# Kernel tuning notes

Measured on AMD Instinct MI355X. Metric: run time of the kernel, lower is better.

The kernel has to match this reference:

```python
import jax, jax.numpy as jnp
import numpy as np
import math

B, S, D = 16, 2048, 128

def setup_inputs() -> dict:
    key = jax.random.key(0)
    k1, k2, k3, k4 = jax.random.split(key, 4)
    query = jax.random.normal(k1, (B, S, D), dtype=jnp.float32)
    key_t = jax.random.normal(k2, (B, S, D), dtype=jnp.float32)
    value = jax.random.normal(k3, (B, S, D), dtype=jnp.float32)
    attn_mask = jax.random.randint(k4, (B, S, S), 0, 2).astype(bool)
    return {"query": query, "key": key_t, "value": value, "attn_mask": attn_mask}

def reference(query, key, value, attn_mask):
    # score = Q K^T / sqrt(d)  -> [B, Sq, Sk]
    scale = 1.0 / math.sqrt(query.shape[-1])
    score = jnp.einsum('bqd,bkd->bqk', query, key) * scale
    # faithful quirk: masked positions are replaced by the VALUE 1e-9 (not -inf)
    mask_score = jnp.where(attn_mask, jnp.float32(1e-9), score)
    # faithful quirk: softmax over dim=1 (the query axis), as in the torch source
    score_matrix = jax.nn.softmax(mask_score, axis=1)
    # output = softmax(scores) @ V  -> [B, Sq, D]
    output = jnp.einsum('bqk,bkd->bqd', score_matrix, value)
    return output
```

## Files before the change

kernel.cpp:

```cpp
#include <hip/hip_runtime.h>
#include <math.h>

#define NB 16
#define SS 2048
#define DQ 128
#define SCALE 0.08838834764831845f

typedef __bf16 bf16x8 __attribute__((ext_vector_type(8)));
typedef unsigned short ushort8_t __attribute__((ext_vector_type(8)));
typedef float floatx4 __attribute__((ext_vector_type(4)));

__device__ __forceinline__ unsigned short f2bf(float x) {
  unsigned int u = __float_as_uint(x);
  u += 0x7fffu + ((u >> 16) & 1u);
  return (unsigned short)(u >> 16);
}
union FragU { ushort8_t u; bf16x8 b; };
__device__ __forceinline__ bf16x8 ld_frag(const unsigned short* p) {
  FragU t; t.u = *(const ushort8_t*)p; return t.b;
}
__device__ __forceinline__ floatx4 mfma16(bf16x8 a, bf16x8 b, floatx4 c) {
  return __builtin_amdgcn_mfma_f32_16x16x32_bf16(a, b, c, 0, 0, 0);
}

__device__ __forceinline__ void bar_lds() {
  asm volatile("s_waitcnt lgkmcnt(0)\n\ts_barrier" ::: "memory");
}


__global__ void zero_accum(float* __restrict__ O) {
  float* p = O + (size_t)blockIdx.x * SS * DQ + 16 * DQ;
#pragma unroll
  for (int i = 0; i < 8; ++i) p[threadIdx.x + 256 * i] = 0.f;
}

template<int WRITE_E>
__global__ __launch_bounds__(256, 4) void pass1_colsum(
    const float* __restrict__ Q, const float* __restrict__ K,
    const int* __restrict__ M, float* __restrict__ O,
    unsigned short* __restrict__ E)
{
  const int k0  = blockIdx.x * 64;
  const int b   = blockIdx.y;
  const int qc  = blockIdx.z;
  const int tid = threadIdx.x;
  const int w = tid >> 6, lane = tid & 63, l15 = lane & 15, quad = lane >> 4;

  __shared__ unsigned short Kbf[64][136];
  __shared__ unsigned short Qbf[64][136];
  __shared__ float red[4][64];

  const float* Qb = Q + (size_t)b * SS * DQ;
  const float* Kb = K + (size_t)b * SS * DQ;
  const int*   Mb = M + (size_t)b * SS * SS;
  unsigned short* Eb = WRITE_E ? (E + (size_t)b * SS * SS) : nullptr;

  const int srow = tid >> 5;
  const int sc4  = (tid & 31) * 4;

#pragma unroll
  for (int r = 0; r < 8; ++r) {
    int row = srow + r * 8;
    float4 v = *(const float4*)(Kb + (size_t)(k0 + row) * DQ + sc4);
    *(ushort4*)&Kbf[row][sc4] = make_ushort4(f2bf(v.x), f2bf(v.y), f2bf(v.z), f2bf(v.w));
  }

  const int qlane = 16 * w + l15;

  float4 qreg[8];
  int4 mv_nxt[4];
  {
    const int q0 = qc * 512;
#pragma unroll
    for (int r = 0; r < 8; ++r)
      qreg[r] = *(const float4*)(Qb + (size_t)(q0 + srow + r * 8) * DQ + sc4);
#pragma unroll
    for (int i = 0; i < 4; ++i)
      mv_nxt[i] = *(const int4*)(Mb + (size_t)(q0 + qlane) * SS + k0 + 16 * i + quad * 4);
  }

  float colacc[16];
#pragma unroll
  for (int t = 0; t < 16; ++t) colacc[t] = 0.f;

  for (int qi = 0; qi < 8; ++qi) {
    bar_lds();
    int4 mv[4] = {mv_nxt[0], mv_nxt[1], mv_nxt[2], mv_nxt[3]};
#pragma unroll
    for (int r = 0; r < 8; ++r) {
      float4 v = qreg[r];
      *(ushort4*)&Qbf[srow + r * 8][sc4] =
          make_ushort4(f2bf(v.x), f2bf(v.y), f2bf(v.z), f2bf(v.w));
    }
    bar_lds();
    if (qi < 7) {
      const int qn = qc * 512 + (qi + 1) * 64;
#pragma unroll
      for (int r = 0; r < 8; ++r)
        qreg[r] = *(const float4*)(Qb + (size_t)(qn + srow + r * 8) * DQ + sc4);
#pragma unroll
      for (int i = 0; i < 4; ++i)
        mv_nxt[i] = *(const int4*)(Mb + (size_t)(qn + qlane) * SS + k0 + 16 * i + quad * 4);
    }

    floatx4 acc[4];
#pragma unroll
    for (int i = 0; i < 4; ++i) acc[i] = (floatx4){0.f, 0.f, 0.f, 0.f};
#pragma unroll
    for (int d0 = 0; d0 < DQ; d0 += 32) {
      bf16x8 bq = ld_frag(&Qbf[qlane][d0 + quad * 8]);
#pragma unroll
      for (int i = 0; i < 4; ++i) {
        bf16x8 ak = ld_frag(&Kbf[16 * i + l15][d0 + quad * 8]);
        acc[i] = mfma16(ak, bq, acc[i]);
      }
    }
    const int qrow = qc * 512 + qi * 64 + qlane;
#pragma unroll
    for (int i = 0; i < 4; ++i) {
      int mm[4] = {mv[i].x, mv[i].y, mv[i].z, mv[i].w};
      float ev[4];
#pragma unroll
      for (int r = 0; r < 4; ++r) {
        float s = mm[r] ? 1e-9f : acc[i][r] * SCALE;
        ev[r] = __expf(s);
        colacc[i * 4 + r] += ev[r];
      }
      if (WRITE_E) {
        *(ushort4*)(Eb + (size_t)qrow * SS + k0 + 16 * i + quad * 4) =
            make_ushort4(f2bf(ev[0]), f2bf(ev[1]), f2bf(ev[2]), f2bf(ev[3]));
      }
    }
  }

#pragma unroll
  for (int t = 0; t < 16; ++t) {
    colacc[t] += __shfl_xor(colacc[t], 1, 64);
    colacc[t] += __shfl_xor(colacc[t], 2, 64);
    colacc[t] += __shfl_xor(colacc[t], 4, 64);
    colacc[t] += __shfl_xor(colacc[t], 8, 64);
  }
  if (l15 == 0) {
#pragma unroll
    for (int i = 0; i < 4; ++i)
#pragma unroll
      for (int r = 0; r < 4; ++r)
        red[w][16 * i + quad * 4 + r] = colacc[i * 4 + r];
  }
  bar_lds();
  if (tid < 64) {
    float s = red[0][tid] + red[1][tid] + red[2][tid] + red[3][tid];
    atomicAdd(O + (size_t)b * SS * DQ + 16 * DQ + k0 + tid, s);
  }
}

__global__ void combine_linv(float* __restrict__ O) {
  const int b  = blockIdx.x;
  const int jb = blockIdx.y * 4;
  float* Ob = O + (size_t)b * SS * DQ;
#pragma unroll
  for (int it = 0; it < 8; ++it) {
    int k = threadIdx.x + 256 * it;
    float inv = 1.0f / Ob[16 * DQ + k];
#pragma unroll
    for (int j = 0; j < 4; ++j)
      Ob[(size_t)(64 * (jb + j)) * DQ + k] = inv;
  }
}

__global__ __launch_bounds__(256, 2) void pass2_pv(
    const float* __restrict__ V, const unsigned short* __restrict__ E,
    float* __restrict__ O)
{
  const int b = blockIdx.y, q0 = blockIdx.x * 64;
  const int tid = threadIdx.x;
  const int w = tid >> 6, lane = tid & 63, l15 = lane & 15, quad = lane >> 4;

  __shared__ unsigned short Wt[128][72];
  __shared__ float Li[SS];

  const float* Vb = V + (size_t)b * SS * DQ;
  const unsigned short* Erow =
      E + (size_t)b * SS * SS + (size_t)(q0 + 16 * w + l15) * SS;

  const int sc4 = (tid & 31) * 4;
  const int vk2 = (tid >> 5) * 2;

  {
    const float* src = O + ((size_t)b * SS + q0) * DQ;
#pragma unroll
    for (int r = 0; r < 2; ++r) {
      int idx = (tid + r * 256) * 4;
      *(float4*)&Li[idx] = *(const float4*)(src + idx);
    }
  }

  floatx4 accO[8];
#pragma unroll
  for (int j = 0; j < 8; ++j) accO[j] = (floatx4){0.f, 0.f, 0.f, 0.f};

  float4 vreg[8];
  FragU ef_nxt[2];
  {
#pragma unroll
    for (int r = 0; r < 4; ++r) {
      int k2 = vk2 + r * 16;
      vreg[2 * r]     = *(const float4*)(Vb + (size_t)(k2)     * DQ + sc4);
      vreg[2 * r + 1] = *(const float4*)(Vb + (size_t)(k2 + 1) * DQ + sc4);
    }
#pragma unroll
    for (int c = 0; c < 2; ++c)
      ef_nxt[c].u = *(const ushort8_t*)(Erow + 32 * c + quad * 8);
  }

  for (int k0 = 0; k0 < SS; k0 += 64) {
    bar_lds();
    FragU ef[2] = {ef_nxt[0], ef_nxt[1]};

#pragma unroll
    for (int r = 0; r < 4; ++r) {
      int k2 = vk2 + r * 16;
      float la = Li[k0 + k2], lb = Li[k0 + k2 + 1];
      float fa[4] = {vreg[2*r].x * la, vreg[2*r].y * la,
                     vreg[2*r].z * la, vreg[2*r].w * la};
      float fb[4] = {vreg[2*r+1].x * lb, vreg[2*r+1].y * lb,
                     vreg[2*r+1].z * lb, vreg[2*r+1].w * lb};
#pragma unroll
      for (int i = 0; i < 4; ++i) {
        int d  = sc4 + i;
        int kk = k2 ^ ((((unsigned)d >> 2) & 7) << 3);
        *(ushort2*)&Wt[d][kk] = make_ushort2(f2bf(fa[i]), f2bf(fb[i]));
      }
    }
    bar_lds();

    if (k0 + 64 < SS) {
      const int kn = k0 + 64;
#pragma unroll
      for (int r = 0; r < 4; ++r) {
        int k2 = vk2 + r * 16;
        vreg[2 * r]     = *(const float4*)(Vb + (size_t)(kn + k2)     * DQ + sc4);
        vreg[2 * r + 1] = *(const float4*)(Vb + (size_t)(kn + k2 + 1) * DQ + sc4);
      }
#pragma unroll
      for (int c = 0; c < 2; ++c)
        ef_nxt[c].u = *(const ushort8_t*)(Erow + kn + 32 * c + quad * 8);
    }

#pragma unroll
    for (int c = 0; c < 2; ++c) {
      bf16x8 be = ef[c].b;
#pragma unroll
      for (int j = 0; j < 8; ++j) {
        int d  = 16 * j + l15;
        int kk = (32 * c + quad * 8) ^ ((((unsigned)d >> 2) & 7) << 3);
        bf16x8 aw = ld_frag(&Wt[d][kk]);
        accO[j] = mfma16(aw, be, accO[j]);
      }
    }
  }

#pragma unroll
  for (int j = 0; j < 8; ++j) {
    float* op = O + ((size_t)b * SS + q0 + 16 * w + l15) * DQ + 16 * j + quad * 4;
    *(float4*)op = make_float4(accO[j][0], accO[j][1], accO[j][2], accO[j][3]);
  }
}

__global__ __launch_bounds__(256, 2) void pass2_out(
    const float* __restrict__ Q, const float* __restrict__ K,
    const float* __restrict__ V, const int* __restrict__ M,
    float* __restrict__ O)
{
  const int b = blockIdx.y, q0 = blockIdx.x * 64;
  const int tid = threadIdx.x;
  const int w = tid >> 6, lane = tid & 63, l15 = lane & 15, quad = lane >> 4;

  __shared__ unsigned short Kbf[64][136];
  __shared__ unsigned short Es[64][72];
  __shared__ unsigned short Wt[128][72];
  __shared__ float Li[SS];

  const float* Qb = Q + (size_t)b * SS * DQ;
  const float* Kb = K + (size_t)b * SS * DQ;
  const float* Vb = V + (size_t)b * SS * DQ;
  const int*   Mb = M + (size_t)b * SS * SS;

  const int srow = tid >> 5;
  const int sc4  = (tid & 31) * 4;

  {
    const float* src = O + ((size_t)b * SS + q0) * DQ;
#pragma unroll
    for (int r = 0; r < 2; ++r) {
      int idx = (tid + r * 256) * 4;
      *(float4*)&Li[idx] = *(const float4*)(src + idx);
    }
  }
  FragU qf[4];
  {
    const float* qrow = Qb + (size_t)(q0 + 16 * w + l15) * DQ;
#pragma unroll
    for (int i = 0; i < 4; ++i) {
      float4 a = *(const float4*)(qrow + 32 * i + quad * 8);
      float4 c = *(const float4*)(qrow + 32 * i + quad * 8 + 4);
      qf[i].u = (ushort8_t){f2bf(a.x), f2bf(a.y), f2bf(a.z), f2bf(a.w),
                            f2bf(c.x), f2bf(c.y), f2bf(c.z), f2bf(c.w)};
    }
  }

  floatx4 accO[8];
#pragma unroll
  for (int j = 0; j < 8; ++j) accO[j] = (floatx4){0.f, 0.f, 0.f, 0.f};

  const int* mrow = Mb + (size_t)(q0 + 16 * w + l15) * SS;

  float4 kreg[8], vreg[8];
  int4 mv_nxt[4];
  const int vk2 = (tid >> 5) * 2;
  {
#pragma unroll
    for (int r = 0; r < 8; ++r)
      kreg[r] = *(const float4*)(Kb + (size_t)(srow + r * 8) * DQ + sc4);
#pragma unroll
    for (int r = 0; r < 4; ++r) {
      int k2 = vk2 + r * 16;
      vreg[2 * r]     = *(const float4*)(Vb + (size_t)(k2)     * DQ + sc4);
      vreg[2 * r + 1] = *(const float4*)(Vb + (size_t)(k2 + 1) * DQ + sc4);
    }
#pragma unroll
    for (int j = 0; j < 4; ++j)
      mv_nxt[j] = *(const int4*)(mrow + 16 * j + quad * 4);
  }

  for (int k0 = 0; k0 < SS; k0 += 64) {
    bar_lds();
    int4 mv[4] = {mv_nxt[0], mv_nxt[1], mv_nxt[2], mv_nxt[3]};

#pragma unroll
    for (int r = 0; r < 8; ++r) {
      float4 v = kreg[r];
      *(ushort4*)&Kbf[srow + r * 8][sc4] =
          make_ushort4(f2bf(v.x), f2bf(v.y), f2bf(v.z), f2bf(v.w));
    }
#pragma unroll
    for (int r = 0; r < 4; ++r) {
      int k2 = vk2 + r * 16;
      float fa[4] = {vreg[2*r].x, vreg[2*r].y, vreg[2*r].z, vreg[2*r].w};
      float fb[4] = {vreg[2*r+1].x, vreg[2*r+1].y, vreg[2*r+1].z, vreg[2*r+1].w};
#pragma unroll
      for (int i = 0; i < 4; ++i) {
        int d  = sc4 + i;
        int kk = k2 ^ ((((unsigned)d >> 2) & 7) << 3);
        *(ushort2*)&Wt[d][kk] = make_ushort2(f2bf(fa[i]), f2bf(fb[i]));
      }
    }
    bar_lds();

    if (k0 + 64 < SS) {
      const int kn = k0 + 64;
#pragma unroll
      for (int r = 0; r < 8; ++r)
        kreg[r] = *(const float4*)(Kb + (size_t)(kn + srow + r * 8) * DQ + sc4);
#pragma unroll
      for (int r = 0; r < 4; ++r) {
        int k2 = vk2 + r * 16;
        vreg[2 * r]     = *(const float4*)(Vb + (size_t)(kn + k2)     * DQ + sc4);
        vreg[2 * r + 1] = *(const float4*)(Vb + (size_t)(kn + k2 + 1) * DQ + sc4);
      }
#pragma unroll
      for (int j = 0; j < 4; ++j)
        mv_nxt[j] = *(const int4*)(mrow + kn + 16 * j + quad * 4);
    }

    floatx4 acc[4];
#pragma unroll
    for (int j = 0; j < 4; ++j) acc[j] = (floatx4){0.f, 0.f, 0.f, 0.f};
#pragma unroll
    for (int i = 0; i < 4; ++i) {
      bf16x8 bq = qf[i].b;
#pragma unroll
      for (int j = 0; j < 4; ++j) {
        bf16x8 ak = ld_frag(&Kbf[16 * j + l15][32 * i + quad * 8]);
        acc[j] = mfma16(ak, bq, acc[j]);
      }
    }
#pragma unroll
    for (int j = 0; j < 4; ++j) {
      float4 liv = *(const float4*)&Li[k0 + 16 * j + quad * 4];
      float lv[4] = {liv.x, liv.y, liv.z, liv.w};
      int mm[4] = {mv[j].x, mv[j].y, mv[j].z, mv[j].w};
      unsigned short es[4];
#pragma unroll
      for (int r = 0; r < 4; ++r) {
        float s = mm[r] ? 1e-9f : acc[j][r] * SCALE;
        es[r] = f2bf(__expf(s) * lv[r]);
      }
      *(ushort4*)&Es[16 * w + l15][16 * j + quad * 4] =
          make_ushort4(es[0], es[1], es[2], es[3]);
    }
#pragma unroll
    for (int c = 0; c < 2; ++c) {
      bf16x8 be = ld_frag(&Es[16 * w + l15][32 * c + quad * 8]);
#pragma unroll
      for (int j = 0; j < 8; ++j) {
        int d  = 16 * j + l15;
        int kk = (32 * c + quad * 8) ^ ((((unsigned)d >> 2) & 7) << 3);
        bf16x8 aw = ld_frag(&Wt[d][kk]);
        accO[j] = mfma16(aw, be, accO[j]);
      }
    }
  }

#pragma unroll
  for (int j = 0; j < 8; ++j) {
    float* op = O + ((size_t)b * SS + q0 + 16 * w + l15) * DQ + 16 * j + quad * 4;
    *(float4*)op = make_float4(accO[j][0], accO[j][1], accO[j][2], accO[j][3]);
  }
}

extern "C" void kernel_launch(void* const* d_in, const int* in_sizes, int n_in,
                              void* d_out, int out_size, void* d_ws, size_t ws_size,
                              hipStream_t stream) {
  const float* Q = (const float*)d_in[0];
  const float* K = (const float*)d_in[1];
  const float* V = (const float*)d_in[2];
  const int*   M = (const int*)d_in[3];
  float* O = (float*)d_out;

  const size_t eneed = (size_t)NB * SS * SS * sizeof(unsigned short);

  zero_accum<<<dim3(NB), 256, 0, stream>>>(O);
  if (d_ws != nullptr && ws_size >= eneed) {
    unsigned short* E = (unsigned short*)d_ws;
    pass1_colsum<1><<<dim3(32, NB, 4), 256, 0, stream>>>(Q, K, M, O, E);
    combine_linv<<<dim3(NB, 8), 256, 0, stream>>>(O);
    pass2_pv<<<dim3(32, NB), 256, 0, stream>>>(V, E, O);
  } else {
    pass1_colsum<0><<<dim3(32, NB, 4), 256, 0, stream>>>(Q, K, M, O, nullptr);
    combine_linv<<<dim3(NB, 8), 256, 0, stream>>>(O);
    pass2_out<<<dim3(32, NB), 256, 0, stream>>>(Q, K, V, M, O);
  }
}
```

Baseline: 513.5 us.

## Split PV pass over two key halves and keep Q fragments in registers

```diff
diff --git a/kernel.cpp b/kernel.cpp
--- a/kernel.cpp
+++ b/kernel.cpp
@@ -47,7 +47,6 @@
   const int w = tid >> 6, lane = tid & 63, l15 = lane & 15, quad = lane >> 4;
 
   __shared__ unsigned short Kbf[64][136];
-  __shared__ unsigned short Qbf[64][136];
   __shared__ float red[4][64];
 
   const float* Qb = Q + (size_t)b * SS * DQ;
@@ -64,70 +63,80 @@
     float4 v = *(const float4*)(Kb + (size_t)(k0 + row) * DQ + sc4);
     *(ushort4*)&Kbf[row][sc4] = make_ushort4(f2bf(v.x), f2bf(v.y), f2bf(v.z), f2bf(v.w));
   }
+  bar_lds();
 
   const int qlane = 16 * w + l15;
+  const float* qrowp = Qb + (size_t)(qc * 512 + qlane) * DQ;
+  const int*   mrowp = Mb + (size_t)(qc * 512 + qlane) * SS + k0;
 
   float4 qreg[8];
   int4 mv_nxt[4];
-  {
-    const int q0 = qc * 512;
-#pragma unroll
-    for (int r = 0; r < 8; ++r)
-      qreg[r] = *(const float4*)(Qb + (size_t)(q0 + srow + r * 8) * DQ + sc4);
-#pragma unroll
-    for (int i = 0; i < 4; ++i)
-      mv_nxt[i] = *(const int4*)(Mb + (size_t)(q0 + qlane) * SS + k0 + 16 * i + quad * 4);
-  }
+#pragma unroll
+  for (int i = 0; i < 4; ++i) {
+    qreg[2 * i]     = *(const float4*)(qrowp + 32 * i + quad * 8);
+    qreg[2 * i + 1] = *(const float4*)(qrowp + 32 * i + quad * 8 + 4);
+  }
+#pragma unroll
+  for (int j = 0; j < 4; ++j)
+    mv_nxt[j] = *(const int4*)(mrowp + 16 * j + quad * 4);
 
   float colacc[16];
 #pragma unroll
   for (int t = 0; t < 16; ++t) colacc[t] = 0.f;
 
   for (int qi = 0; qi < 8; ++qi) {
-    bar_lds();
-    int4 mv[4] = {mv_nxt[0], mv_nxt[1], mv_nxt[2], mv_nxt[3]};
-#pragma unroll
-    for (int r = 0; r < 8; ++r) {
-      float4 v = qreg[r];
-      *(ushort4*)&Qbf[srow + r * 8][sc4] =
-          make_ushort4(f2bf(v.x), f2bf(v.y), f2bf(v.z), f2bf(v.w));
-    }
-    bar_lds();
+    FragU qf[4];
+#pragma unroll
+    for (int i = 0; i < 4; ++i) {
+      float4 a = qreg[2 * i], c = qreg[2 * i + 1];
+      qf[i].u = (ushort8_t){f2bf(a.x), f2bf(a.y), f2bf(a.z), f2bf(a.w),
+                            f2bf(c.x), f2bf(c.y), f2bf(c.z), f2bf(c.w)};
+    }
+    int mbits = 0;
+#pragma unroll
+    for (int j = 0; j < 4; ++j) {
+      mbits |= (mv_nxt[j].x ? 1 : 0) << (4 * j + 0);
+      mbits |= (mv_nxt[j].y ? 1 : 0) << (4 * j + 1);
+      mbits |= (mv_nxt[j].z ? 1 : 0) << (4 * j + 2);
+      mbits |= (mv_nxt[j].w ? 1 : 0) << (4 * j + 3);
+    }
     if (qi < 7) {
-      const int qn = qc * 512 + (qi + 1) * 64;
-#pragma unroll
-      for (int r = 0; r < 8; ++r)
-        qreg[r] = *(const float4*)(Qb + (size_t)(qn + srow + r * 8) * DQ + sc4);
-#pragma unroll
-      for (int i = 0; i < 4; ++i)
-        mv_nxt[i] = *(const int4*)(Mb + (size_t)(qn + qlane) * SS + k0 + 16 * i + quad * 4);
+      const float* qp = qrowp + (size_t)(qi + 1) * 64 * DQ;
+      const int*   mp = mrowp + (size_t)(qi + 1) * 64 * SS;
+#pragma unroll
+      for (int i = 0; i < 4; ++i) {
+        qreg[2 * i]     = *(const float4*)(qp + 32 * i + quad * 8);
+        qreg[2 * i + 1] = *(const float4*)(qp + 32 * i + quad * 8 + 4);
+      }
+#pragma unroll
+      for (int j = 0; j < 4; ++j)
+        mv_nxt[j] = *(const int4*)(mp + 16 * j + quad * 4);
     }
 
     floatx4 acc[4];
 #pragma unroll
-    for (int i = 0; i < 4; ++i) acc[i] = (floatx4){0.f, 0.f, 0.f, 0.f};
-#pragma unroll
-    for (int d0 = 0; d0 < DQ; d0 += 32) {
-      bf16x8 bq = ld_frag(&Qbf[qlane][d0 + quad * 8]);
-#pragma unroll
-      for (int i = 0; i < 4; ++i) {
-        bf16x8 ak = ld_frag(&Kbf[16 * i + l15][d0 + quad * 8]);
-        acc[i] = mfma16(ak, bq, acc[i]);
+    for (int j = 0; j < 4; ++j) acc[j] = (floatx4){0.f, 0.f, 0.f, 0.f};
+#pragma unroll
+    for (int i = 0; i < 4; ++i) {
+      bf16x8 bq = qf[i].b;
+#pragma unroll
+      for (int j = 0; j < 4; ++j) {
+        bf16x8 ak = ld_frag(&Kbf[16 * j + l15][32 * i + quad * 8]);
+        acc[j] = mfma16(ak, bq, acc[j]);
       }
     }
     const int qrow = qc * 512 + qi * 64 + qlane;
 #pragma unroll
-    for (int i = 0; i < 4; ++i) {
-      int mm[4] = {mv[i].x, mv[i].y, mv[i].z, mv[i].w};
+    for (int j = 0; j < 4; ++j) {
       float ev[4];
 #pragma unroll
       for (int r = 0; r < 4; ++r) {
-        float s = mm[r] ? 1e-9f : acc[i][r] * SCALE;
+        float s = ((mbits >> (4 * j + r)) & 1) ? 1e-9f : acc[j][r] * SCALE;
         ev[r] = __expf(s);
-        colacc[i * 4 + r] += ev[r];
+        colacc[j * 4 + r] += ev[r];
       }
       if (WRITE_E) {
-        *(ushort4*)(Eb + (size_t)qrow * SS + k0 + 16 * i + quad * 4) =
+        *(ushort4*)(Eb + (size_t)qrow * SS + k0 + 16 * j + quad * 4) =
             make_ushort4(f2bf(ev[0]), f2bf(ev[1]), f2bf(ev[2]), f2bf(ev[3]));
       }
     }
@@ -168,31 +177,29 @@
   }
 }
 
-__global__ __launch_bounds__(256, 2) void pass2_pv(
+__global__ __launch_bounds__(256, 4) void pass2_pv(
     const float* __restrict__ V, const unsigned short* __restrict__ E,
-    float* __restrict__ O)
+    const float* __restrict__ O, float* __restrict__ P)
 {
-  const int b = blockIdx.y, q0 = blockIdx.x * 64;
+  const int b = blockIdx.z, q0 = blockIdx.x * 64, kh = blockIdx.y;
+  const int kbase = kh * (SS / 2);
   const int tid = threadIdx.x;
   const int w = tid >> 6, lane = tid & 63, l15 = lane & 15, quad = lane >> 4;
 
   __shared__ unsigned short Wt[128][72];
-  __shared__ float Li[SS];
+  __shared__ float Li[SS / 2];
 
   const float* Vb = V + (size_t)b * SS * DQ;
   const unsigned short* Erow =
-      E + (size_t)b * SS * SS + (size_t)(q0 + 16 * w + l15) * SS;
+      E + (size_t)b * SS * SS + (size_t)(q0 + 16 * w + l15) * SS + kbase;
 
   const int sc4 = (tid & 31) * 4;
   const int vk2 = (tid >> 5) * 2;
 
   {
-    const float* src = O + ((size_t)b * SS + q0) * DQ;
-#pragma unroll
-    for (int r = 0; r < 2; ++r) {
-      int idx = (tid + r * 256) * 4;
-      *(float4*)&Li[idx] = *(const float4*)(src + idx);
-    }
+    const float* src = O + ((size_t)b * SS + q0) * DQ + kbase;
+    int idx = tid * 4;
+    *(float4*)&Li[idx] = *(const float4*)(src + idx);
   }
 
   floatx4 accO[8];
@@ -205,15 +212,15 @@
 #pragma unroll
     for (int r = 0; r < 4; ++r) {
       int k2 = vk2 + r * 16;
-      vreg[2 * r]     = *(const float4*)(Vb + (size_t)(k2)     * DQ + sc4);
-      vreg[2 * r + 1] = *(const float4*)(Vb + (size_t)(k2 + 1) * DQ + sc4);
+      vreg[2 * r]     = *(const float4*)(Vb + (size_t)(kbase + k2)     * DQ + sc4);
+      vreg[2 * r + 1] = *(const float4*)(Vb + (size_t)(kbase + k2 + 1) * DQ + sc4);
     }
 #pragma unroll
     for (int c = 0; c < 2; ++c)
       ef_nxt[c].u = *(const ushort8_t*)(Erow + 32 * c + quad * 8);
   }
 
-  for (int k0 = 0; k0 < SS; k0 += 64) {
+  for (int k0 = 0; k0 < SS / 2; k0 += 64) {
     bar_lds();
     FragU ef[2] = {ef_nxt[0], ef_nxt[1]};
 
@@ -234,13 +241,13 @@
     }
     bar_lds();
 
-    if (k0 + 64 < SS) {
+    if (k0 + 64 < SS / 2) {
       const int kn = k0 + 64;
 #pragma unroll
       for (int r = 0; r < 4; ++r) {
         int k2 = vk2 + r * 16;
-        vreg[2 * r]     = *(const float4*)(Vb + (size_t)(kn + k2)     * DQ + sc4);
-        vreg[2 * r + 1] = *(const float4*)(Vb + (size_t)(kn + k2 + 1) * DQ + sc4);
+        vreg[2 * r]     = *(const float4*)(Vb + (size_t)(kbase + kn + k2)     * DQ + sc4);
+        vreg[2 * r + 1] = *(const float4*)(Vb + (size_t)(kbase + kn + k2 + 1) * DQ + sc4);
       }
 #pragma unroll
       for (int c = 0; c < 2; ++c)
@@ -262,8 +269,23 @@
 
 #pragma unroll
   for (int j = 0; j < 8; ++j) {
-    float* op = O + ((size_t)b * SS + q0 + 16 * w + l15) * DQ + 16 * j + quad * 4;
+    float* op = P + (((size_t)(kh * NB + b) * SS) + q0 + 16 * w + l15) * DQ
+                  + 16 * j + quad * 4;
     *(float4*)op = make_float4(accO[j][0], accO[j][1], accO[j][2], accO[j][3]);
+  }
+}
+
+__global__ void combine_O(const float* __restrict__ P, float* __restrict__ O) {
+  const size_t boff = (size_t)blockIdx.x * SS * DQ + (size_t)blockIdx.y * 8192;
+  const float* P0 = P + boff;
+  const float* P1 = P + (size_t)NB * SS * DQ + boff;
+  float* Ob = O + boff;
+#pragma unroll
+  for (int it = 0; it < 8; ++it) {
+    int i = (threadIdx.x + 256 * it) * 4;
+    float4 a = *(const float4*)(P0 + i);
+    float4 c = *(const float4*)(P1 + i);
+    *(float4*)(Ob + i) = make_float4(a.x + c.x, a.y + c.y, a.z + c.z, a.w + c.w);
   }
 }
 
@@ -429,13 +451,16 @@
   float* O = (float*)d_out;
 
   const size_t eneed = (size_t)NB * SS * SS * sizeof(unsigned short);
+  const size_t pneed = eneed + (size_t)2 * NB * SS * DQ * sizeof(float);
 
   zero_accum<<<dim3(NB), 256, 0, stream>>>(O);
-  if (d_ws != nullptr && ws_size >= eneed) {
+  if (d_ws != nullptr && ws_size >= pneed) {
     unsigned short* E = (unsigned short*)d_ws;
+    float* P = (float*)((char*)d_ws + eneed);
     pass1_colsum<1><<<dim3(32, NB, 4), 256, 0, stream>>>(Q, K, M, O, E);
     combine_linv<<<dim3(NB, 8), 256, 0, stream>>>(O);
-    pass2_pv<<<dim3(32, NB), 256, 0, stream>>>(V, E, O);
+    pass2_pv<<<dim3(32, 2, NB), 256, 0, stream>>>(V, E, O, P);
+    combine_O<<<dim3(NB, 32), 256, 0, stream>>>(P, O);
   } else {
     pass1_colsum<0><<<dim3(32, NB, 4), 256, 0, stream>>>(Q, K, M, O, nullptr);
     combine_linv<<<dim3(NB, 8), 256, 0, stream>>>(O);
```

Measured after the change: 603.8 us. +17.6%, slower.

## Split PV pass over key halves and fuse reciprocal into PV load

Applied to the files above, without the earlier changes.

```diff
diff --git a/kernel.cpp b/kernel.cpp
--- a/kernel.cpp
+++ b/kernel.cpp
@@ -168,31 +168,33 @@
   }
 }
 
-__global__ __launch_bounds__(256, 2) void pass2_pv(
+__global__ __launch_bounds__(256, 4) void pass2_pv(
     const float* __restrict__ V, const unsigned short* __restrict__ E,
-    float* __restrict__ O)
+    const float* __restrict__ O, float* __restrict__ P)
 {
-  const int b = blockIdx.y, q0 = blockIdx.x * 64;
+  const int b = blockIdx.z, q0 = blockIdx.x * 64, kh = blockIdx.y;
+  const int kbase = kh * (SS / 2);
   const int tid = threadIdx.x;
   const int w = tid >> 6, lane = tid & 63, l15 = lane & 15, quad = lane >> 4;
 
   __shared__ unsigned short Wt[128][72];
-  __shared__ float Li[SS];
+  __shared__ float Li[SS / 2];
 
   const float* Vb = V + (size_t)b * SS * DQ;
   const unsigned short* Erow =
-      E + (size_t)b * SS * SS + (size_t)(q0 + 16 * w + l15) * SS;
+      E + (size_t)b * SS * SS + (size_t)(q0 + 16 * w + l15) * SS + kbase;
 
   const int sc4 = (tid & 31) * 4;
   const int vk2 = (tid >> 5) * 2;
 
   {
-    const float* src = O + ((size_t)b * SS + q0) * DQ;
-#pragma unroll
-    for (int r = 0; r < 2; ++r) {
-      int idx = (tid + r * 256) * 4;
-      *(float4*)&Li[idx] = *(const float4*)(src + idx);
-    }
+    const float* src = O + (size_t)b * SS * DQ + 16 * DQ + kbase;
+    int idx = tid * 4;
+    float4 c = *(const float4*)(src + idx);
+    Li[idx + 0] = 1.0f / c.x;
+    Li[idx + 1] = 1.0f / c.y;
+    Li[idx + 2] = 1.0f / c.z;
+    Li[idx + 3] = 1.0f / c.w;
   }
 
   floatx4 accO[8];
@@ -205,15 +207,15 @@
 #pragma unroll
     for (int r = 0; r < 4; ++r) {
       int k2 = vk2 + r * 16;
-      vreg[2 * r]     = *(const float4*)(Vb + (size_t)(k2)     * DQ + sc4);
-      vreg[2 * r + 1] = *(const float4*)(Vb + (size_t)(k2 + 1) * DQ + sc4);
+      vreg[2 * r]     = *(const float4*)(Vb + (size_t)(kbase + k2)     * DQ + sc4);
+      vreg[2 * r + 1] = *(const float4*)(Vb + (size_t)(kbase + k2 + 1) * DQ + sc4);
     }
 #pragma unroll
     for (int c = 0; c < 2; ++c)
       ef_nxt[c].u = *(const ushort8_t*)(Erow + 32 * c + quad * 8);
   }
 
-  for (int k0 = 0; k0 < SS; k0 += 64) {
+  for (int k0 = 0; k0 < SS / 2; k0 += 64) {
     bar_lds();
     FragU ef[2] = {ef_nxt[0], ef_nxt[1]};
 
@@ -234,13 +236,13 @@
     }
     bar_lds();
 
-    if (k0 + 64 < SS) {
+    if (k0 + 64 < SS / 2) {
       const int kn = k0 + 64;
 #pragma unroll
       for (int r = 0; r < 4; ++r) {
         int k2 = vk2 + r * 16;
-        vreg[2 * r]     = *(const float4*)(Vb + (size_t)(kn + k2)     * DQ + sc4);
-        vreg[2 * r + 1] = *(const float4*)(Vb + (size_t)(kn + k2 + 1) * DQ + sc4);
+        vreg[2 * r]     = *(const float4*)(Vb + (size_t)(kbase + kn + k2)     * DQ + sc4);
+        vreg[2 * r + 1] = *(const float4*)(Vb + (size_t)(kbase + kn + k2 + 1) * DQ + sc4);
       }
 #pragma unroll
       for (int c = 0; c < 2; ++c)
@@ -262,8 +264,23 @@
 
 #pragma unroll
   for (int j = 0; j < 8; ++j) {
-    float* op = O + ((size_t)b * SS + q0 + 16 * w + l15) * DQ + 16 * j + quad * 4;
+    float* op = P + (((size_t)(kh * NB + b) * SS) + q0 + 16 * w + l15) * DQ
+                  + 16 * j + quad * 4;
     *(float4*)op = make_float4(accO[j][0], accO[j][1], accO[j][2], accO[j][3]);
+  }
+}
+
+__global__ void combine_O(const float* __restrict__ P, float* __restrict__ O) {
+  const size_t boff = (size_t)blockIdx.x * SS * DQ + (size_t)blockIdx.y * 8192;
+  const float* P0 = P + boff;
+  const float* P1 = P + (size_t)NB * SS * DQ + boff;
+  float* Ob = O + boff;
+#pragma unroll
+  for (int it = 0; it < 8; ++it) {
+    int i = (threadIdx.x + 256 * it) * 4;
+    float4 a = *(const float4*)(P0 + i);
+    float4 c = *(const float4*)(P1 + i);
+    *(float4*)(Ob + i) = make_float4(a.x + c.x, a.y + c.y, a.z + c.z, a.w + c.w);
   }
 }
 
@@ -429,13 +446,15 @@
   float* O = (float*)d_out;
 
   const size_t eneed = (size_t)NB * SS * SS * sizeof(unsigned short);
+  const size_t pneed = eneed + (size_t)2 * NB * SS * DQ * sizeof(float);
 
   zero_accum<<<dim3(NB), 256, 0, stream>>>(O);
-  if (d_ws != nullptr && ws_size >= eneed) {
+  if (d_ws != nullptr && ws_size >= pneed) {
     unsigned short* E = (unsigned short*)d_ws;
+    float* P = (float*)((char*)d_ws + eneed);
     pass1_colsum<1><<<dim3(32, NB, 4), 256, 0, stream>>>(Q, K, M, O, E);
-    combine_linv<<<dim3(NB, 8), 256, 0, stream>>>(O);
-    pass2_pv<<<dim3(32, NB), 256, 0, stream>>>(V, E, O);
+    pass2_pv<<<dim3(32, 2, NB), 256, 0, stream>>>(V, E, O, P);
+    combine_O<<<dim3(NB, 32), 256, 0, stream>>>(P, O);
   } else {
     pass1_colsum<0><<<dim3(32, NB, 4), 256, 0, stream>>>(Q, K, M, O, nullptr);
     combine_linv<<<dim3(NB, 8), 256, 0, stream>>>(O);
```

New measurement: 524.1 us. 1.02x slower.

## Swap pass1 loop to keep Q fragments in registers and stream K tiles

Applied to the files above, without the earlier changes.

```diff
diff --git a/kernel.cpp b/kernel.cpp
--- a/kernel.cpp
+++ b/kernel.cpp
@@ -40,117 +40,113 @@
     const int* __restrict__ M, float* __restrict__ O,
     unsigned short* __restrict__ E)
 {
-  const int k0  = blockIdx.x * 64;
+  const int qs  = blockIdx.x * 64;
   const int b   = blockIdx.y;
-  const int qc  = blockIdx.z;
+  const int kc0 = blockIdx.z * 512;
   const int tid = threadIdx.x;
   const int w = tid >> 6, lane = tid & 63, l15 = lane & 15, quad = lane >> 4;
 
   __shared__ unsigned short Kbf[64][136];
-  __shared__ unsigned short Qbf[64][136];
-  __shared__ float red[4][64];
-
-  const float* Qb = Q + (size_t)b * SS * DQ;
+  __shared__ float Csum[4][512];
+
   const float* Kb = K + (size_t)b * SS * DQ;
-  const int*   Mb = M + (size_t)b * SS * SS;
-  unsigned short* Eb = WRITE_E ? (E + (size_t)b * SS * SS) : nullptr;
+  const int qrow = qs + 16 * w + l15;
+
+  const int*   mrow = M + (size_t)b * SS * SS + (size_t)qrow * SS + kc0;
+  unsigned short* Ep =
+      WRITE_E ? (E + (size_t)b * SS * SS + (size_t)qrow * SS + kc0) : nullptr;
 
   const int srow = tid >> 5;
   const int sc4  = (tid & 31) * 4;
 
-#pragma unroll
-  for (int r = 0; r < 8; ++r) {
-    int row = srow + r * 8;
-    float4 v = *(const float4*)(Kb + (size_t)(k0 + row) * DQ + sc4);
-    *(ushort4*)&Kbf[row][sc4] = make_ushort4(f2bf(v.x), f2bf(v.y), f2bf(v.z), f2bf(v.w));
-  }
-
-  const int qlane = 16 * w + l15;
-
-  float4 qreg[8];
+  FragU qf[4];
+  {
+    const float* qp = Q + (size_t)b * SS * DQ + (size_t)qrow * DQ;
+#pragma unroll
+    for (int i = 0; i < 4; ++i) {
+      float4 a = *(const float4*)(qp + 32 * i + quad * 8);
+      float4 c = *(const float4*)(qp + 32 * i + quad * 8 + 4);
+      qf[i].u = (ushort8_t){f2bf(a.x), f2bf(a.y), f2bf(a.z), f2bf(a.w),
+                            f2bf(c.x), f2bf(c.y), f2bf(c.z), f2bf(c.w)};
+    }
+  }
+
+#pragma unroll
+  for (int t = 0; t < 8; ++t) Csum[w][lane + 64 * t] = 0.f;
+
+  float4 kreg[8];
   int4 mv_nxt[4];
-  {
-    const int q0 = qc * 512;
-#pragma unroll
-    for (int r = 0; r < 8; ++r)
-      qreg[r] = *(const float4*)(Qb + (size_t)(q0 + srow + r * 8) * DQ + sc4);
-#pragma unroll
-    for (int i = 0; i < 4; ++i)
-      mv_nxt[i] = *(const int4*)(Mb + (size_t)(q0 + qlane) * SS + k0 + 16 * i + quad * 4);
-  }
-
-  float colacc[16];
-#pragma unroll
-  for (int t = 0; t < 16; ++t) colacc[t] = 0.f;
-
-  for (int qi = 0; qi < 8; ++qi) {
+#pragma unroll
+  for (int r = 0; r < 8; ++r)
+    kreg[r] = *(const float4*)(Kb + (size_t)(kc0 + srow + r * 8) * DQ + sc4);
+#pragma unroll
+  for (int j = 0; j < 4; ++j)
+    mv_nxt[j] = *(const int4*)(mrow + 16 * j + quad * 4);
+
+  for (int kt = 0; kt < 8; ++kt) {
+    const int kbl = kt * 64;
     bar_lds();
     int4 mv[4] = {mv_nxt[0], mv_nxt[1], mv_nxt[2], mv_nxt[3]};
 #pragma unroll
     for (int r = 0; r < 8; ++r) {
-      float4 v = qreg[r];
-      *(ushort4*)&Qbf[srow + r * 8][sc4] =
+      float4 v = kreg[r];
+      *(ushort4*)&Kbf[srow + r * 8][sc4] =
           make_ushort4(f2bf(v.x), f2bf(v.y), f2bf(v.z), f2bf(v.w));
     }
     bar_lds();
-    if (qi < 7) {
-      const int qn = qc * 512 + (qi + 1) * 64;
+    if (kt < 7) {
+      const int kn = kbl + 64;
 #pragma unroll
       for (int r = 0; r < 8; ++r)
-        qreg[r] = *(const float4*)(Qb + (size_t)(qn + srow + r * 8) * DQ + sc4);
-#pragma unroll
-      for (int i = 0; i < 4; ++i)
-        mv_nxt[i] = *(const int4*)(Mb + (size_t)(qn + qlane) * SS + k0 + 16 * i + quad * 4);
+        kreg[r] = *(const float4*)(Kb + (size_t)(kc0 + kn + srow + r * 8) * DQ + sc4);
+#pragma unroll
+      for (int j = 0; j < 4; ++j)
+        mv_nxt[j] = *(const int4*)(mrow + kn + 16 * j + quad * 4);
     }
 
     floatx4 acc[4];
 #pragma unroll
-    for (int i = 0; i < 4; ++i) acc[i] = (floatx4){0.f, 0.f, 0.f, 0.f};
-#pragma unroll
-    for (int d0 = 0; d0 < DQ; d0 += 32) {
-      bf16x8 bq = ld_frag(&Qbf[qlane][d0 + quad * 8]);
-#pragma unroll
-      for (int i = 0; i < 4; ++i) {
-        bf16x8 ak = ld_frag(&Kbf[16 * i + l15][d0 + quad * 8]);
-        acc[i] = mfma16(ak, bq, acc[i]);
-      }
-    }
-    const int qrow = qc * 512 + qi * 64 + qlane;
+    for (int j = 0; j < 4; ++j) acc[j] = (floatx4){0.f, 0.f, 0.f, 0.f};
 #pragma unroll
     for (int i = 0; i < 4; ++i) {
-      int mm[4] = {mv[i].x, mv[i].y, mv[i].z, mv[i].w};
+      bf16x8 bq = qf[i].b;
+#pragma unroll
+      for (int j = 0; j < 4; ++j) {
+        bf16x8 ak = ld_frag(&Kbf[16 * j + l15][32 * i + quad * 8]);
+        acc[j] = mfma16(ak, bq, acc[j]);
+      }
+    }
+#pragma unroll
+    for (int j = 0; j < 4; ++j) {
+      int mm[4] = {mv[j].x, mv[j].y, mv[j].z, mv[j].w};
       float ev[4];
 #pragma unroll
       for (int r = 0; r < 4; ++r) {
-        float s = mm[r] ? 1e-9f : acc[i][r] * SCALE;
+        float s = mm[r] ? 1e-9f : acc[j][r] * SCALE;
         ev[r] = __expf(s);
-        colacc[i * 4 + r] += ev[r];
       }
       if (WRITE_E) {
-        *(ushort4*)(Eb + (size_t)qrow * SS + k0 + 16 * i + quad * 4) =
+        *(ushort4*)(Ep + kbl + 16 * j + quad * 4) =
             make_ushort4(f2bf(ev[0]), f2bf(ev[1]), f2bf(ev[2]), f2bf(ev[3]));
       }
-    }
-  }
-
-#pragma unroll
-  for (int t = 0; t < 16; ++t) {
-    colacc[t] += __shfl_xor(colacc[t], 1, 64);
-    colacc[t] += __shfl_xor(colacc[t], 2, 64);
-    colacc[t] += __shfl_xor(colacc[t], 4, 64);
-    colacc[t] += __shfl_xor(colacc[t], 8, 64);
-  }
-  if (l15 == 0) {
-#pragma unroll
-    for (int i = 0; i < 4; ++i)
-#pragma unroll
-      for (int r = 0; r < 4; ++r)
-        red[w][16 * i + quad * 4 + r] = colacc[i * 4 + r];
-  }
+#pragma unroll
+      for (int r = 0; r < 4; ++r) {
+        float c = ev[r];
+        c += __shfl_xor(c, 1, 64);
+        c += __shfl_xor(c, 2, 64);
+        c += __shfl_xor(c, 4, 64);
+        c += __shfl_xor(c, 8, 64);
+        if (l15 == 0) Csum[w][kbl + 16 * j + quad * 4 + r] += c;
+      }
+    }
+  }
+
   bar_lds();
-  if (tid < 64) {
-    float s = red[0][tid] + red[1][tid] + red[2][tid] + red[3][tid];
-    atomicAdd(O + (size_t)b * SS * DQ + 16 * DQ + k0 + tid, s);
+#pragma unroll
+  for (int t = 0; t < 2; ++t) {
+    int k = tid + 256 * t;
+    float s = Csum[0][k] + Csum[1][k] + Csum[2][k] + Csum[3][k];
+    atomicAdd(O + (size_t)b * SS * DQ + 16 * DQ + kc0 + k, s);
   }
 }
 
```

Result: slower. 533.5 us (+3.9%).
